# Performance work log

Hardware: AMD Instinct MI355X
Metric: run time of the kernel (lower is better)

## Reference

```python
import jax, jax.numpy as jnp
import numpy as np

DIM = 1024
HEADS = 16
DIM_HEAD = 64
INNER = HEADS * DIM_HEAD
ALPHA = 128.0
SCALE = DIM_HEAD ** -0.5 / ALPHA
EPS = 1e-5
MAX_NEG = -jnp.finfo(jnp.float32).max


def layernorm(x, g):
    # torch.var(unbiased=False) layernorm with learned gain, no bias
    mean = jnp.mean(x, axis=-1, keepdims=True)
    var = jnp.mean(jnp.square(x - mean), axis=-1, keepdims=True)
    return (x - mean) * jax.lax.rsqrt(var + EPS) * g


def setup_inputs() -> dict:
    key = jax.random.key(0)
    ks = jax.random.split(key, 8)
    b, n = 8, 1024
    x = jax.random.normal(ks[0], (b, n, DIM), dtype=jnp.float32)
    mask = jax.random.bernoulli(ks[1], 0.9, (b, n))  # bool padding mask
    g_in = jnp.ones((DIM,), jnp.float32)
    Wq = jax.random.normal(ks[2], (INNER, DIM), jnp.float32) * (DIM ** -0.5)
    Wkv = jax.random.normal(ks[3], (2 * DIM_HEAD, DIM), jnp.float32) * (DIM ** -0.5)
    null_kv = jax.random.normal(ks[4], (2, DIM_HEAD), jnp.float32)
    Wo = jax.random.normal(ks[5], (DIM, INNER), jnp.float32) * (INNER ** -0.5)
    g_out = jnp.ones((DIM,), jnp.float32)
    return {"x": x, "mask": mask, "g_in": g_in, "Wq": Wq, "Wkv": Wkv,
            "null_kv": null_kv, "Wo": Wo, "g_out": g_out}


def reference(x, mask, g_in, Wq, Wkv, null_kv, Wo, g_out):
    b, n, _ = x.shape
    context = x                      # context captured BEFORE norm
    xn = layernorm(x, g_in)
    q = (xn @ Wq.T).reshape(b, n, HEADS, DIM_HEAD).transpose(0, 2, 1, 3)  # b h n d
    q = q * SCALE
    kv = context @ Wkv.T             # b n 2d (single shared KV head: MQA)
    k, v = jnp.split(kv, 2, axis=-1)
    nk = jnp.broadcast_to(null_kv[0], (b, 1, DIM_HEAD))
    nv = jnp.broadcast_to(null_kv[1], (b, 1, DIM_HEAD))
    k = jnp.concatenate([nk, k], axis=1)   # b (n+1) d
    v = jnp.concatenate([nv, v], axis=1)
    sim = jnp.einsum('bhid,bjd->bhij', q, k)  # b h n (n+1)
    # padding mask, True prepended for null token
    m = jnp.pad(mask, ((0, 0), (1, 0)), constant_values=True)
    sim = jnp.where(m[:, None, None, :], sim, MAX_NEG)
    # causal mask: triu with offset j-i+1 = 2 (null token always visible)
    i, j = n, n + 1
    causal = jnp.triu(jnp.ones((i, j), bool), j - i + 1)
    sim = jnp.where(causal, MAX_NEG, sim)
    # pb-relax: subtract detached max, rescale by alpha, softmax
    sim = sim - jax.lax.stop_gradient(jnp.max(sim, axis=-1, keepdims=True))
    attn = jax.nn.softmax(sim * ALPHA, axis=-1)
    out = jnp.einsum('bhij,bjd->bhid', attn, v)
    out = out.transpose(0, 2, 1, 3).reshape(b, n, INNER)
    out = out @ Wo.T
    return layernorm(out, g_out)
```

## Files before the change

kernel.cpp:

```cpp
#include <hip/hip_runtime.h>
#include <hip/hip_bf16.h>

#define B_     8
#define N_     1024
#define DIM_   1024
#define HEADS_ 16
#define DH_    64
#define INNER_ 1024
#define NKEY_  1025
#define NTILE_ 34
#define NW_    34
#define ROWS_  8192
#define EPS_   1e-5f
#define QK_SCALE_ 0.1803368801111f
#define TILE_ELEMS_ 4096

typedef unsigned short u16;
typedef unsigned char  u8;
typedef unsigned int   u32;
typedef __attribute__((ext_vector_type(8)))  short bf16x8;
typedef __attribute__((ext_vector_type(4)))  float f32x4;
typedef __attribute__((ext_vector_type(16))) float f32x16;

__device__ __forceinline__ float bf2f(u16 u) {
    unsigned int x = ((unsigned int)u) << 16;
    return __uint_as_float(x);
}
__device__ __forceinline__ u16 f2bf(float f) {
    unsigned int x = __float_as_uint(f);
    x += 0x7FFFu + ((x >> 16) & 1u);
    return (u16)(x >> 16);
}
__device__ __forceinline__ float exp2fast(float x) {
    float r;
    asm("v_exp_f32 %0, %1" : "=v"(r) : "v"(x));
    return r;
}

#define MFMA16(a, b, c) __builtin_amdgcn_mfma_f32_16x16x32_bf16((a), (b), (c), 0, 0, 0)
#define MFMA32(a, b, c) __builtin_amdgcn_mfma_f32_32x32x16_bf16((a), (b), (c), 0, 0, 0)

__device__ __forceinline__ void gload16(const void* g, void* l) {
    __builtin_amdgcn_global_load_lds(
        (const __attribute__((address_space(1))) unsigned int*)g,
        (__attribute__((address_space(3))) unsigned int*)l, 16, 0, 0);
}

__device__ __forceinline__ u32 cvtpk(float lo, float hi) {
    u32 r;
    asm("v_cvt_pk_bf16_f32 %0, %1, %2" : "=v"(r) : "v"(lo), "v"(hi));
    return r;
}
__device__ __forceinline__ void plswap(u32& a, u32& b) {
    asm volatile("v_permlane32_swap_b32 %0, %1" : "+v"(a), "+v"(b));
}

__global__ void detect_mask(const unsigned int* __restrict__ m, int* __restrict__ flag) {
    if (threadIdx.x == 0 && blockIdx.x == 0) {
        int f = 0;
        for (int i = 0; i < 64; ++i) {
            unsigned int w = m[i];
            if (w == 0x3F800000u) { f = 2; break; }
            if (w > 1u) f = 1;
        }
        *flag = f;
    }
}

__global__ void build_bits(const void* __restrict__ mraw, const int* __restrict__ flag,
                           u32* __restrict__ vbits) {
    int tid = blockIdx.x * blockDim.x + threadIdx.x;
    if (tid >= B_ * NW_) return;
    int b = tid / NW_, wq = tid - b * NW_;
    int f = *flag;
    u32 bits = 0;
    for (int i = 0; i < 32; ++i) {
        int jp = wq * 32 + i;
        bool vis;
        if (jp == 0) vis = true;
        else if (jp < NKEY_) {
            int idx = b * N_ + jp - 1;
            if (f == 0)      vis = ((const int*)mraw)[idx] != 0;
            else if (f == 1) vis = ((const u8*)mraw)[idx] != 0;
            else             vis = ((const float*)mraw)[idx] != 0.0f;
        } else vis = false;
        if (vis) bits |= (1u << i);
    }
    vbits[tid] = bits;
}

__global__ void cvt_w(const float* __restrict__ wq, const float* __restrict__ wkv,
                      const float* __restrict__ wo, u16* __restrict__ q16,
                      u16* __restrict__ kv16, u16* __restrict__ o16) {
    int i = blockIdx.x * blockDim.x + threadIdx.x;
    const int NQ = INNER_ * DIM_ / 4, NKV = 128 * DIM_ / 4, NO = DIM_ * INNER_ / 4;
    const float* src; u16* dst; int off;
    if (i < NQ)            { src = wq;  dst = q16;  off = i; }
    else if (i < NQ + NKV) { src = wkv; dst = kv16; off = i - NQ; }
    else if (i < NQ + NKV + NO) { src = wo; dst = o16; off = i - NQ - NKV; }
    else return;
    float4 v = ((const float4*)src)[off];
    ushort4 u; u.x = f2bf(v.x); u.y = f2bf(v.y); u.z = f2bf(v.z); u.w = f2bf(v.w);
    ((ushort4*)dst)[off] = u;
}

template<int MODE>
__global__ __launch_bounds__(256)
void ln_rows(const void* __restrict__ xv, const float* __restrict__ g,
             void* __restrict__ outv, u16* __restrict__ raw16) {
    int row = blockIdx.x;
    int t = threadIdx.x;
    float v0, v1, v2, v3;
    if constexpr (MODE == 0) {
        float4 v = ((const float4*)((const float*)xv + (size_t)row * DIM_))[t];
        v0 = v.x; v1 = v.y; v2 = v.z; v3 = v.w;
    } else {
        ushort4 u = ((const ushort4*)((const u16*)xv + (size_t)row * DIM_))[t];
        v0 = bf2f(u.x); v1 = bf2f(u.y); v2 = bf2f(u.z); v3 = bf2f(u.w);
    }
    float s  = v0 + v1 + v2 + v3;
    float ss = v0*v0 + v1*v1 + v2*v2 + v3*v3;
#pragma unroll
    for (int off = 32; off > 0; off >>= 1) {
        s  += __shfl_down(s,  off, 64);
        ss += __shfl_down(ss, off, 64);
    }
    __shared__ float red[10];
    int wid = t >> 6, lane = t & 63;
    if (lane == 0) { red[wid] = s; red[4 + wid] = ss; }
    __syncthreads();
    if (t == 0) {
        float S  = red[0] + red[1] + red[2] + red[3];
        float SS = red[4] + red[5] + red[6] + red[7];
        float mean = S * (1.0f / DIM_);
        float var  = SS * (1.0f / DIM_) - mean * mean;
        red[8] = mean;
        red[9] = rsqrtf(var + EPS_);
    }
    __syncthreads();
    float mean = red[8], rs = red[9];
    float4 gv = ((const float4*)g)[t];
    float o0 = (v0 - mean) * rs * gv.x;
    float o1 = (v1 - mean) * rs * gv.y;
    float o2 = (v2 - mean) * rs * gv.z;
    float o3 = (v3 - mean) * rs * gv.w;
    if constexpr (MODE == 0) {
        ushort4 u; u.x = f2bf(o0); u.y = f2bf(o1); u.z = f2bf(o2); u.w = f2bf(o3);
        ((ushort4*)((u16*)outv + (size_t)row * DIM_))[t] = u;
        ushort4 rw; rw.x = f2bf(v0); rw.y = f2bf(v1); rw.z = f2bf(v2); rw.w = f2bf(v3);
        ((ushort4*)(raw16 + (size_t)row * DIM_))[t] = rw;
    } else {
        float4 u; u.x = o0; u.y = o1; u.z = o2; u.w = o3;
        ((float4*)((float*)outv + (size_t)row * DIM_))[t] = u;
    }
}

__global__ __launch_bounds__(256)
void proj_fused(const u16* __restrict__ xn, const u16* __restrict__ xraw,
                const u16* __restrict__ wq, const u16* __restrict__ wkv,
                u16* __restrict__ qout, float* __restrict__ kvout) {
    __shared__ u16 As[128 * 32];
    __shared__ u16 Bs[128 * 32];
    const bool iskv = (blockIdx.x == 8);
    const u16* A  = iskv ? xraw : xn;
    const u16* Bt = iskv ? wkv : wq;
    const int  n0 = iskv ? 0 : blockIdx.x * 128;
    const float scale = iskv ? 1.0f : QK_SCALE_;
    const int t = threadIdx.x;
    const int w = t >> 6, l = t & 63;
    const int col = l & 15, rg = l >> 4;
    const int wm = (w >> 1) * 64, wn = (w & 1) * 64;
    const int m0 = blockIdx.y * 128;
    const int slr = l >> 2;
    const int slc = (l & 3) * 8;
    f32x4 acc[4][4];
#pragma unroll
    for (int i = 0; i < 4; ++i)
#pragma unroll
        for (int j = 0; j < 4; ++j) acc[i][j] = f32x4{0.f, 0.f, 0.f, 0.f};

    const u16* Abase = A  + (size_t)m0 * DIM_;
    const u16* Bbase = Bt + (size_t)n0 * DIM_;
    for (int k0 = 0; k0 < DIM_; k0 += 32) {
        __syncthreads();
#pragma unroll
        for (int p = 0; p < 2; ++p) {
            int rb = w * 2 + p;
            gload16(Abase + (size_t)(rb * 16 + slr) * DIM_ + k0 + slc, &As[rb * 512]);
            gload16(Bbase + (size_t)(rb * 16 + slr) * DIM_ + k0 + slc, &Bs[rb * 512]);
        }
        __syncthreads();
        bf16x8 af[4], bf4[4];
#pragma unroll
        for (int mi = 0; mi < 4; ++mi)
            af[mi] = *(const bf16x8*)&As[(wm + mi * 16 + col) * 32 + rg * 8];
#pragma unroll
        for (int ni = 0; ni < 4; ++ni)
            bf4[ni] = *(const bf16x8*)&Bs[(wn + ni * 16 + col) * 32 + rg * 8];
#pragma unroll
        for (int mi = 0; mi < 4; ++mi)
#pragma unroll
            for (int ni = 0; ni < 4; ++ni)
                acc[mi][ni] = MFMA16(af[mi], bf4[ni], acc[mi][ni]);
    }
#pragma unroll
    for (int mi = 0; mi < 4; ++mi)
#pragma unroll
        for (int ni = 0; ni < 4; ++ni)
#pragma unroll
            for (int r = 0; r < 4; ++r) {
                size_t row = (size_t)(m0 + wm + mi * 16 + rg * 4 + r);
                int c = n0 + wn + ni * 16 + col;
                float vv = acc[mi][ni][r] * scale;
                if (iskv) kvout[row * 128 + c] = vv;
                else      qout[row * INNER_ + c] = f2bf(vv);
            }
}

__global__ __launch_bounds__(256)
void gemm_o(const u16* __restrict__ A, const u16* __restrict__ Bt,
            u16* __restrict__ Cv) {
    __shared__ u16 As[128 * 32];
    __shared__ u16 Bs[128 * 32];
    const int t = threadIdx.x;
    const int w = t >> 6, l = t & 63;
    const int col = l & 15, rg = l >> 4;
    const int wm = (w >> 1) * 64, wn = (w & 1) * 64;
    const int m0 = blockIdx.y * 128, n0 = blockIdx.x * 128;
    const int slr = l >> 2;
    const int slc = (l & 3) * 8;
    f32x4 acc[4][4];
#pragma unroll
    for (int i = 0; i < 4; ++i)
#pragma unroll
        for (int j = 0; j < 4; ++j) acc[i][j] = f32x4{0.f, 0.f, 0.f, 0.f};
    const u16* Abase = A  + (size_t)m0 * INNER_;
    const u16* Bbase = Bt + (size_t)n0 * INNER_;
    for (int k0 = 0; k0 < INNER_; k0 += 32) {
        __syncthreads();
#pragma unroll
        for (int p = 0; p < 2; ++p) {
            int rb = w * 2 + p;
            gload16(Abase + (size_t)(rb * 16 + slr) * INNER_ + k0 + slc, &As[rb * 512]);
            gload16(Bbase + (size_t)(rb * 16 + slr) * INNER_ + k0 + slc, &Bs[rb * 512]);
        }
        __syncthreads();
        bf16x8 af[4], bf4[4];
#pragma unroll
        for (int mi = 0; mi < 4; ++mi)
            af[mi] = *(const bf16x8*)&As[(wm + mi * 16 + col) * 32 + rg * 8];
#pragma unroll
        for (int ni = 0; ni < 4; ++ni)
            bf4[ni] = *(const bf16x8*)&Bs[(wn + ni * 16 + col) * 32 + rg * 8];
#pragma unroll
        for (int mi = 0; mi < 4; ++mi)
#pragma unroll
            for (int ni = 0; ni < 4; ++ni)
                acc[mi][ni] = MFMA16(af[mi], bf4[ni], acc[mi][ni]);
    }
#pragma unroll
    for (int mi = 0; mi < 4; ++mi)
#pragma unroll
        for (int ni = 0; ni < 4; ++ni)
#pragma unroll
            for (int r = 0; r < 4; ++r) {
                size_t row = (size_t)(m0 + wm + mi * 16 + rg * 4 + r);
                int c = n0 + wn + ni * 16 + col;
                Cv[row * DIM_ + c] = f2bf(acc[mi][ni][r]);
            }
}

__global__ __launch_bounds__(256)
void build_kv(const float* __restrict__ kvf, const float* __restrict__ nullkv,
              u16* __restrict__ KVt) {
    const int kt = blockIdx.x, b = blockIdx.y;
    const int t = threadIdx.x;
    const int k0 = kt * 32;
    u16* base = KVt + ((size_t)b * NTILE_ + kt) * TILE_ELEMS_;
    {
        int j = t >> 3;
        int d0 = (t & 7) * 8;
        int jp = k0 + j;
        float v[8];
        if (jp == 0) {
#pragma unroll
            for (int i = 0; i < 8; ++i) v[i] = nullkv[d0 + i];
        } else if (jp <= N_) {
            const float* r = kvf + ((size_t)b * N_ + jp - 1) * 128 + d0;
            float4 a = ((const float4*)r)[0], c = ((const float4*)r)[1];
            v[0]=a.x; v[1]=a.y; v[2]=a.z; v[3]=a.w; v[4]=c.x; v[5]=c.y; v[6]=c.z; v[7]=c.w;
        } else {
#pragma unroll
            for (int i = 0; i < 8; ++i) v[i] = 0.f;
        }
        ushort4 u0, u1;
        u0.x=f2bf(v[0]); u0.y=f2bf(v[1]); u0.z=f2bf(v[2]); u0.w=f2bf(v[3]);
        u1.x=f2bf(v[4]); u1.y=f2bf(v[5]); u1.z=f2bf(v[6]); u1.w=f2bf(v[7]);
        *(ushort4*)(base + j * 64 + d0)     = u0;
        *(ushort4*)(base + j * 64 + d0 + 4) = u1;
    }
    {
        int d = t >> 2;
        int j0 = (t & 3) * 8;
        u16 o8[8];
#pragma unroll
        for (int i = 0; i < 8; ++i) {
            int jp = k0 + j0 + i;
            float val = 0.f;
            if (jp == 0) val = nullkv[64 + d];
            else if (jp <= N_) val = kvf[((size_t)b * N_ + jp - 1) * 128 + 64 + d];
            o8[i] = f2bf(val);
        }
        u16* dst = base + 2048 + d * 32 + j0;
        ushort4 u0, u1;
        u0.x=o8[0]; u0.y=o8[1]; u0.z=o8[2]; u0.w=o8[3];
        u1.x=o8[4]; u1.y=o8[5]; u1.z=o8[6]; u1.w=o8[7];
        *(ushort4*)dst = u0;
        *(ushort4*)(dst + 4) = u1;
    }
}

__global__ __launch_bounds__(256)
void attn_un(const u16* __restrict__ Q, const u16* __restrict__ KVt,
             const u32* __restrict__ vbits, u16* __restrict__ Out) {
    const int t = threadIdx.x;
    const int w = t >> 6, l = t & 63;
    const int lo = l & 31, hi = l >> 5;
    const int fid = blockIdx.x;
    const int qt = 31 - (fid >> 5);
    const int rem = fid & 31;
    const int b = rem >> 2, hg = rem & 3;
    const int h = hg * 4 + w;
    const int i0 = qt * 32;
    const int nst = (qt + 3) >> 1;

    bf16x8 qf[4];
    {
        const u16* qp = Q + ((size_t)(b * N_ + i0 + lo)) * INNER_ + h * DH_ + hi * 8;
#pragma unroll
        for (int dt = 0; dt < 4; ++dt) qf[dt] = *(const bf16x8*)(qp + dt * 16);
    }
    f32x16 o0, o1, lacc;
#pragma unroll
    for (int i = 0; i < 16; ++i) { o0[i] = 0.f; o1[i] = 0.f; lacc[i] = 0.f; }

    union { u32 wd[4]; bf16x8 v; } onesA;
    onesA.wd[0] = 0x3F803F80u; onesA.wd[1] = 0x3F803F80u;
    onesA.wd[2] = 0x3F803F80u; onesA.wd[3] = 0x3F803F80u;

    const u16* tbase = KVt + (size_t)b * NTILE_ * TILE_ELEMS_;
    const u32* vbp = vbits + b * NW_;
    const int koff  = lo * 64 + hi * 8;
    const int voff0 = 2048 + lo * 32 + hi * 8;
    const int voff1 = 2048 + (lo + 32) * 32 + hi * 8;

    for (int st = 0; st < nst; ++st) {
        const int kt0 = st * 2, kt1 = st * 2 + 1;
        const u16* tb0 = tbase + (size_t)kt0 * TILE_ELEMS_;
        const u16* tb1 = tbase + (size_t)kt1 * TILE_ELEMS_;
        bf16x8 kf0[4], kf1[4];
        kf0[0] = *(const bf16x8*)(tb0 + koff);
        kf0[1] = *(const bf16x8*)(tb0 + koff + 16);
        kf0[2] = *(const bf16x8*)(tb0 + koff + 32);
        kf0[3] = *(const bf16x8*)(tb0 + koff + 48);
        kf1[0] = *(const bf16x8*)(tb1 + koff);
        kf1[1] = *(const bf16x8*)(tb1 + koff + 16);
        kf1[2] = *(const bf16x8*)(tb1 + koff + 32);
        kf1[3] = *(const bf16x8*)(tb1 + koff + 48);

        u32 vb0 = vbp[kt0], vb1 = vbp[kt1];
        union { u32 wd[4]; bf16x8 v; } bias0, bias1, ones;
        bias0.wd[0] = (hi == 0 && !((vb0 >> lo) & 1u)) ? 0xC6E0u : 0u;
        bias0.wd[1] = 0; bias0.wd[2] = 0; bias0.wd[3] = 0;
        bias1.wd[0] = (hi == 0 && !((vb1 >> lo) & 1u)) ? 0xC6E0u : 0u;
        bias1.wd[1] = 0; bias1.wd[2] = 0; bias1.wd[3] = 0;
        ones.wd[0] = (hi == 0) ? 0x3F80u : 0u;
        ones.wd[1] = 0; ones.wd[2] = 0; ones.wd[3] = 0;

        f32x16 s0, s1;
        __builtin_amdgcn_s_setprio(1);
#pragma unroll
        for (int i = 0; i < 16; ++i) { s0[i] = 0.f; s1[i] = 0.f; }
        s0 = MFMA32(kf0[0], qf[0], s0);
        s1 = MFMA32(kf1[0], qf[0], s1);
        s0 = MFMA32(kf0[1], qf[1], s0);
        s1 = MFMA32(kf1[1], qf[1], s1);
        s0 = MFMA32(kf0[2], qf[2], s0);
        s1 = MFMA32(kf1[2], qf[2], s1);
        s0 = MFMA32(kf0[3], qf[3], s0);
        s1 = MFMA32(kf1[3], qf[3], s1);
        s0 = MFMA32(bias0.v, ones.v, s0);
        s1 = MFMA32(bias1.v, ones.v, s1);
        __builtin_amdgcn_s_setprio(0);

        float p0[16], p1[16];
#pragma unroll
        for (int r = 0; r < 16; ++r) p0[r] = exp2fast(s0[r]);
#pragma unroll
        for (int r = 0; r < 16; ++r) p1[r] = exp2fast(s1[r]);
        if (kt0 >= qt) {
            int lim0 = i0 + lo + 1 - kt0 * 32 - 4 * hi;
#pragma unroll
            for (int r = 0; r < 16; ++r)
                if (((r & 3) + 8 * (r >> 2)) > lim0) p0[r] = 0.f;
        }
        if (kt1 >= qt) {
            int lim1 = i0 + lo + 1 - kt1 * 32 - 4 * hi;
#pragma unroll
            for (int r = 0; r < 16; ++r)
                if (((r & 3) + 8 * (r >> 2)) > lim1) p1[r] = 0.f;
        }

        u32 a0 = cvtpk(p0[0],  p0[1]),  a2 = cvtpk(p0[4],  p0[5]);  plswap(a0, a2);
        u32 a1 = cvtpk(p0[2],  p0[3]),  a3 = cvtpk(p0[6],  p0[7]);  plswap(a1, a3);
        u32 a4 = cvtpk(p0[8],  p0[9]),  a6 = cvtpk(p0[12], p0[13]); plswap(a4, a6);
        u32 a5 = cvtpk(p0[10], p0[11]), a7 = cvtpk(p0[14], p0[15]); plswap(a5, a7);
        u32 c0 = cvtpk(p1[0],  p1[1]),  c2 = cvtpk(p1[4],  p1[5]);  plswap(c0, c2);
        u32 c1 = cvtpk(p1[2],  p1[3]),  c3 = cvtpk(p1[6],  p1[7]);  plswap(c1, c3);
        u32 c4 = cvtpk(p1[8],  p1[9]),  c6 = cvtpk(p1[12], p1[13]); plswap(c4, c6);
        u32 c5 = cvtpk(p1[10], p1[11]), c7 = cvtpk(p1[14], p1[15]); plswap(c5, c7);
        union { u32 wd[4]; bf16x8 v; } f0, f1, g0, g1;
        f0.wd[0] = a0; f0.wd[1] = a1; f0.wd[2] = a2; f0.wd[3] = a3;
        f1.wd[0] = a4; f1.wd[1] = a5; f1.wd[2] = a6; f1.wd[3] = a7;
        g0.wd[0] = c0; g0.wd[1] = c1; g0.wd[2] = c2; g0.wd[3] = c3;
        g1.wd[0] = c4; g1.wd[1] = c5; g1.wd[2] = c6; g1.wd[3] = c7;

        bf16x8 vf0[4], vf1[4];
        vf0[0] = *(const bf16x8*)(tb0 + voff0);
        vf0[1] = *(const bf16x8*)(tb0 + voff0 + 16);
        vf0[2] = *(const bf16x8*)(tb0 + voff1);
        vf0[3] = *(const bf16x8*)(tb0 + voff1 + 16);
        vf1[0] = *(const bf16x8*)(tb1 + voff0);
        vf1[1] = *(const bf16x8*)(tb1 + voff0 + 16);
        vf1[2] = *(const bf16x8*)(tb1 + voff1);
        vf1[3] = *(const bf16x8*)(tb1 + voff1 + 16);
        __builtin_amdgcn_s_setprio(1);
        o0 = MFMA32(vf0[0], f0.v, o0);
        o1 = MFMA32(vf0[2], f0.v, o1);
        lacc = MFMA32(onesA.v, f0.v, lacc);
        o0 = MFMA32(vf0[1], f1.v, o0);
        o1 = MFMA32(vf0[3], f1.v, o1);
        lacc = MFMA32(onesA.v, f1.v, lacc);
        o0 = MFMA32(vf1[0], g0.v, o0);
        o1 = MFMA32(vf1[2], g0.v, o1);
        lacc = MFMA32(onesA.v, g0.v, lacc);
        o0 = MFMA32(vf1[1], g1.v, o0);
        o1 = MFMA32(vf1[3], g1.v, o1);
        lacc = MFMA32(onesA.v, g1.v, lacc);
        __builtin_amdgcn_s_setprio(0);
    }

    float inv = 1.0f / lacc[0];
    u16* ob = Out + ((size_t)(b * N_ + i0 + lo)) * INNER_ + h * DH_;
#pragma unroll
    for (int dd = 0; dd < 2; ++dd)
#pragma unroll
        for (int g = 0; g < 4; ++g) {
            int d0 = dd * 32 + 8 * g + 4 * hi;
            float e0 = (dd ? o1[4*g+0] : o0[4*g+0]) * inv;
            float e1 = (dd ? o1[4*g+1] : o0[4*g+1]) * inv;
            float e2 = (dd ? o1[4*g+2] : o0[4*g+2]) * inv;
            float e3 = (dd ? o1[4*g+3] : o0[4*g+3]) * inv;
            ushort4 u; u.x = f2bf(e0); u.y = f2bf(e1); u.z = f2bf(e2); u.w = f2bf(e3);
            *(ushort4*)(ob + d0) = u;
        }
}

extern "C" void kernel_launch(void* const* d_in, const int* in_sizes, int n_in,
                              void* d_out, int out_size, void* d_ws, size_t ws_size,
                              hipStream_t stream) {
    const float* x       = (const float*)d_in[0];
    const void*  maskraw = d_in[1];
    const float* g_in    = (const float*)d_in[2];
    const float* Wq      = (const float*)d_in[3];
    const float* Wkv     = (const float*)d_in[4];
    const float* nullkv  = (const float*)d_in[5];
    const float* Wo      = (const float*)d_in[6];
    const float* g_out   = (const float*)d_in[7];
    float* out = (float*)d_out;

    char* ws = (char*)d_ws;
    size_t off = 0;
    auto alloc = [&](size_t bytes) {
        void* p = ws + off;
        off += (bytes + 255) & ~(size_t)255;
        return p;
    };
    int* flag   = (int*)alloc(4);
    u32* vbits  = (u32*)alloc((size_t)B_ * NW_ * 4);
    u16* wq16   = (u16*)alloc((size_t)INNER_ * DIM_ * 2);
    u16* wkv16  = (u16*)alloc((size_t)128 * DIM_ * 2);
    u16* wo16   = (u16*)alloc((size_t)DIM_ * INNER_ * 2);
    u16* bufA   = (u16*)alloc((size_t)ROWS_ * DIM_ * 2);
    u16* xb     = (u16*)alloc((size_t)ROWS_ * DIM_ * 2);
    u16* bufC   = (u16*)alloc((size_t)ROWS_ * INNER_ * 2);
    float* kvf  = (float*)alloc((size_t)ROWS_ * 128 * 4);
    u16* KVt    = (u16*)alloc((size_t)B_ * NTILE_ * TILE_ELEMS_ * 2);

    detect_mask<<<1, 64, 0, stream>>>((const unsigned int*)maskraw, flag);
    build_bits<<<2, 256, 0, stream>>>(maskraw, flag, vbits);

    cvt_w<<<2176, 256, 0, stream>>>(Wq, Wkv, Wo, wq16, wkv16, wo16);

    ln_rows<0><<<ROWS_, 256, 0, stream>>>(x, g_in, bufA, xb);

    proj_fused<<<dim3(9, ROWS_ / 128), 256, 0, stream>>>(
        bufA, xb, wq16, wkv16, bufC, kvf);

    build_kv<<<dim3(NTILE_, B_), 256, 0, stream>>>(kvf, nullkv, KVt);

    attn_un<<<1024, 256, 0, stream>>>(bufC, KVt, vbits, bufA);

    gemm_o<<<dim3(DIM_ / 128, ROWS_ / 128), 256, 0, stream>>>(bufA, wo16, bufC);

    ln_rows<1><<<ROWS_, 256, 0, stream>>>(bufC, g_out, out, nullptr);
}
```

Baseline: 170.2 us.

## Split attention key range across two blocks and combine partials

Splits each query tile's key loop into two halves handled by separate blocks (split-K / flash-decoding style), writing unnormalized bf16 partial outputs and row sums. A new combine kernel adds the partials and normalizes. This doubles grid size to improve occupancy and load balance for the causal triangle, at the cost of extra partial-output memory traffic, an extra launch, and bf16 rounding of unnormalized partials.

After: 186.7 us. 1.1x slower.

```diff
diff --git a/kernel.cpp b/kernel.cpp
--- a/kernel.cpp
+++ b/kernel.cpp
@@ -321,18 +321,24 @@
 }
 
 __global__ __launch_bounds__(256)
-void attn_un(const u16* __restrict__ Q, const u16* __restrict__ KVt,
-             const u32* __restrict__ vbits, u16* __restrict__ Out) {
+void attn_part(const u16* __restrict__ Q, const u16* __restrict__ KVt,
+               const u32* __restrict__ vbits, u16* __restrict__ P0,
+               u16* __restrict__ P1, float* __restrict__ lsums) {
     const int t = threadIdx.x;
     const int w = t >> 6, l = t & 63;
     const int lo = l & 31, hi = l >> 5;
     const int fid = blockIdx.x;
-    const int qt = 31 - (fid >> 5);
-    const int rem = fid & 31;
+    const int split = fid & 1;
+    const int g2 = fid >> 1;
+    const int qt = 31 - (g2 >> 5);
+    const int rem = g2 & 31;
     const int b = rem >> 2, hg = rem & 3;
     const int h = hg * 4 + w;
     const int i0 = qt * 32;
-    const int nst = (qt + 3) >> 1;
+    const int S  = (qt + 3) >> 1;
+    const int S0 = (S + 1) >> 1;
+    const int st_beg = split ? S0 : 0;
+    const int st_end = split ? S : S0;
 
     bf16x8 qf[4];
     {
@@ -354,7 +360,7 @@
     const int voff0 = 2048 + lo * 32 + hi * 8;
     const int voff1 = 2048 + (lo + 32) * 32 + hi * 8;
 
-    for (int st = 0; st < nst; ++st) {
+    for (int st = st_beg; st < st_end; ++st) {
         const int kt0 = st * 2, kt1 = st * 2 + 1;
         const u16* tb0 = tbase + (size_t)kt0 * TILE_ELEMS_;
         const u16* tb1 = tbase + (size_t)kt1 * TILE_ELEMS_;
@@ -450,20 +456,50 @@
         __builtin_amdgcn_s_setprio(0);
     }
 
-    float inv = 1.0f / lacc[0];
-    u16* ob = Out + ((size_t)(b * N_ + i0 + lo)) * INNER_ + h * DH_;
+    u16* opart = (split ? P1 : P0);
+    u16* ob = opart + ((size_t)(b * N_ + i0 + lo)) * INNER_ + h * DH_;
 #pragma unroll
     for (int dd = 0; dd < 2; ++dd)
 #pragma unroll
         for (int g = 0; g < 4; ++g) {
             int d0 = dd * 32 + 8 * g + 4 * hi;
-            float e0 = (dd ? o1[4*g+0] : o0[4*g+0]) * inv;
-            float e1 = (dd ? o1[4*g+1] : o0[4*g+1]) * inv;
-            float e2 = (dd ? o1[4*g+2] : o0[4*g+2]) * inv;
-            float e3 = (dd ? o1[4*g+3] : o0[4*g+3]) * inv;
+            float e0 = (dd ? o1[4*g+0] : o0[4*g+0]);
+            float e1 = (dd ? o1[4*g+1] : o0[4*g+1]);
+            float e2 = (dd ? o1[4*g+2] : o0[4*g+2]);
+            float e3 = (dd ? o1[4*g+3] : o0[4*g+3]);
             ushort4 u; u.x = f2bf(e0); u.y = f2bf(e1); u.z = f2bf(e2); u.w = f2bf(e3);
             *(ushort4*)(ob + d0) = u;
         }
+    if (hi == 0)
+        lsums[(size_t)split * ROWS_ * HEADS_ +
+              (size_t)(b * N_ + i0 + lo) * HEADS_ + h] = lacc[0];
+}
+
+__global__ __launch_bounds__(256)
+void attn_combine(const u16* __restrict__ P0, const u16* __restrict__ P1,
+                  const float* __restrict__ lsums, u16* __restrict__ Out) {
+    int idx = blockIdx.x * 256 + threadIdx.x;
+    size_t base = (size_t)idx * 8;
+    int row = idx >> 7;
+    int h   = (idx >> 3) & 15;
+    float l0 = lsums[(size_t)row * HEADS_ + h];
+    float l1 = lsums[(size_t)ROWS_ * HEADS_ + (size_t)row * HEADS_ + h];
+    float inv = 1.0f / (l0 + l1);
+    ushort4 a0 = *(const ushort4*)(P0 + base);
+    ushort4 a1 = *(const ushort4*)(P0 + base + 4);
+    ushort4 b0 = *(const ushort4*)(P1 + base);
+    ushort4 b1 = *(const ushort4*)(P1 + base + 4);
+    ushort4 u0, u1;
+    u0.x = f2bf((bf2f(a0.x) + bf2f(b0.x)) * inv);
+    u0.y = f2bf((bf2f(a0.y) + bf2f(b0.y)) * inv);
+    u0.z = f2bf((bf2f(a0.z) + bf2f(b0.z)) * inv);
+    u0.w = f2bf((bf2f(a0.w) + bf2f(b0.w)) * inv);
+    u1.x = f2bf((bf2f(a1.x) + bf2f(b1.x)) * inv);
+    u1.y = f2bf((bf2f(a1.y) + bf2f(b1.y)) * inv);
+    u1.z = f2bf((bf2f(a1.z) + bf2f(b1.z)) * inv);
+    u1.w = f2bf((bf2f(a1.w) + bf2f(b1.w)) * inv);
+    *(ushort4*)(Out + base)     = u0;
+    *(ushort4*)(Out + base + 4) = u1;
 }
 
 extern "C" void kernel_launch(void* const* d_in, const int* in_sizes, int n_in,
@@ -486,16 +522,18 @@
         off += (bytes + 255) & ~(size_t)255;
         return p;
     };
-    int* flag   = (int*)alloc(4);
-    u32* vbits  = (u32*)alloc((size_t)B_ * NW_ * 4);
-    u16* wq16   = (u16*)alloc((size_t)INNER_ * DIM_ * 2);
-    u16* wkv16  = (u16*)alloc((size_t)128 * DIM_ * 2);
-    u16* wo16   = (u16*)alloc((size_t)DIM_ * INNER_ * 2);
-    u16* bufA   = (u16*)alloc((size_t)ROWS_ * DIM_ * 2);
-    u16* xb     = (u16*)alloc((size_t)ROWS_ * DIM_ * 2);
-    u16* bufC   = (u16*)alloc((size_t)ROWS_ * INNER_ * 2);
-    float* kvf  = (float*)alloc((size_t)ROWS_ * 128 * 4);
-    u16* KVt    = (u16*)alloc((size_t)B_ * NTILE_ * TILE_ELEMS_ * 2);
+    int* flag    = (int*)alloc(4);
+    u32* vbits   = (u32*)alloc((size_t)B_ * NW_ * 4);
+    u16* wq16    = (u16*)alloc((size_t)INNER_ * DIM_ * 2);
+    u16* wkv16   = (u16*)alloc((size_t)128 * DIM_ * 2);
+    u16* wo16    = (u16*)alloc((size_t)DIM_ * INNER_ * 2);
+    u16* bufA    = (u16*)alloc((size_t)ROWS_ * DIM_ * 2);
+    u16* xb      = (u16*)alloc((size_t)ROWS_ * DIM_ * 2);
+    u16* bufC    = (u16*)alloc((size_t)ROWS_ * INNER_ * 2);
+    float* kvf   = (float*)alloc((size_t)ROWS_ * 128 * 4);
+    u16* KVt     = (u16*)alloc((size_t)B_ * NTILE_ * TILE_ELEMS_ * 2);
+    u16* opart1  = (u16*)alloc((size_t)ROWS_ * INNER_ * 2);
+    float* lsums = (float*)alloc((size_t)2 * ROWS_ * HEADS_ * 4);
 
     detect_mask<<<1, 64, 0, stream>>>((const unsigned int*)maskraw, flag);
     build_bits<<<2, 256, 0, stream>>>(maskraw, flag, vbits);
@@ -509,7 +547,8 @@
 
     build_kv<<<dim3(NTILE_, B_), 256, 0, stream>>>(kvf, nullkv, KVt);
 
-    attn_un<<<1024, 256, 0, stream>>>(bufC, KVt, vbits, bufA);
+    attn_part<<<2048, 256, 0, stream>>>(bufC, KVt, vbits, xb, opart1, lsums);
+    attn_combine<<<4096, 256, 0, stream>>>(xb, opart1, lsums, bufA);
 
     gemm_o<<<dim3(DIM_ / 128, ROWS_ / 128), 256, 0, stream>>>(bufA, wo16, bufC);
 
```
